# Kernel tuning notes

Measured on AMD Instinct MI355X. Metric: run time of the kernel, lower is better.

## Reference

```python
import jax, jax.numpy as jnp
import numpy as np

IN_CHANS = 64
OUT_CHANS = 64
IN_SHAPE = (128, 128)
RADIUS_CUTOFF = 0.03
KERNEL_SHAPE = (3, 4)  # (n_rings, n_phi) -> (3-1)*4+1 = 9 basis functions
EPS = 1e-5
NEG_SLOPE = 0.2


def _disco_basis():
    """Dynamically compile the DISCO filter basis on the (2H, 2W) equidistant grid.

    Returns psi of shape [K, kh, kw] (K=9 hat-function basis filters, including
    quadrature weight hx*hy) plus the pixel radii (Ry, Rx) of the support.
    All static -> constant-folded under jit.
    """
    H2, W2 = 2 * IN_SHAPE[0], 2 * IN_SHAPE[1]
    r_cut = RADIUS_CUTOFF / 2.0
    hy, hx = 1.0 / H2, 1.0 / W2            # normalized grid spacing
    Ry = int(np.ceil(r_cut / hy))
    Rx = int(np.ceil(r_cut / hx))
    dy = np.arange(-Ry, Ry + 1)[:, None] * hy
    dx = np.arange(-Rx, Rx + 1)[None, :] * hx
    r = np.sqrt(dy * dy + dx * dx)
    phi = np.arctan2(dy, dx) % (2.0 * np.pi)
    nr, nphi = KERNEL_SHAPE
    K = (nr - 1) * nphi + 1
    dr = r_cut / (nr - 1)
    dphi = 2.0 * np.pi / nphi
    ik = np.arange(K)[:, None, None]
    ir = np.where(ik > 0, (ik - 1) // nphi + 1, 0)   # radial ring index
    iphi = (ik - 1) % nphi                            # angular index
    # radial hat functions centered at ir*dr, clipped at the cutoff radius
    r_val = np.where((np.abs(r - ir * dr) <= dr) & (r <= r_cut),
                     1.0 - np.abs(r - ir * dr) / dr, 0.0)
    # periodic angular hat functions centered at iphi*dphi
    d_ang = np.abs(phi - iphi * dphi)
    d_ang = np.minimum(d_ang, 2.0 * np.pi - d_ang)
    phi_val = np.where(d_ang <= dphi, 1.0 - d_ang / dphi, 0.0)
    psi = np.where(ik == 0, r_val, r_val * phi_val)   # center basis is isotropic
    psi = psi * (hx * hy)                              # quadrature weight
    return jnp.asarray(psi, jnp.float32), Ry, Rx


def _upsample2x_align_corners(x):
    """Bilinear 2x upsample with align_corners=True, x: [N, C, H, W]."""
    N, C, H, W = x.shape

    def axis(n):
        no = 2 * n
        s = jnp.arange(no, dtype=jnp.float32) * (n - 1) / (no - 1)
        i0 = jnp.floor(s).astype(jnp.int32)
        i1 = jnp.minimum(i0 + 1, n - 1)
        w = (s - i0).astype(x.dtype)
        return i0, i1, w

    y0, y1, wy = axis(H)
    x = x[:, :, y0, :] * (1.0 - wy)[None, None, :, None] + x[:, :, y1, :] * wy[None, None, :, None]
    x0, x1, wx = axis(W)
    x = x[:, :, :, x0] * (1.0 - wx) + x[:, :, :, x1] * wx
    return x


def setup_inputs() -> dict:
    key = jax.random.key(0)
    k1, k2 = jax.random.split(key)
    image = jax.random.normal(k1, (4, IN_CHANS, IN_SHAPE[0], IN_SHAPE[1]), dtype=jnp.float32)
    K = (KERNEL_SHAPE[0] - 1) * KERNEL_SHAPE[1] + 1
    scale = 1.0 / np.sqrt(IN_CHANS * K)
    weight = jax.random.normal(k2, (OUT_CHANS, IN_CHANS, K), dtype=jnp.float32) * scale
    return {"image": image, "weight": weight}


def reference(image, weight):
    x = _upsample2x_align_corners(image)  # [N, Cin, 2H, 2W]
    # 2) DISCO conv: contract learned weights with compiled basis -> dense filter
    psi, Ry, Rx = _disco_basis()          # [K, kh, kw]
    kernel = jnp.einsum('oik,khw->oihw', weight, psi)
    y = jax.lax.conv_general_dilated(
        x, kernel, window_strides=(1, 1),
        padding=[(Ry, Ry), (Rx, Rx)],       # 'constant' zero padding, same size
        dimension_numbers=('NCHW', 'OIHW', 'NCHW'))
    # 3) InstanceNorm2d (affine=False, biased variance, eps=1e-5)
    mu = jnp.mean(y, axis=(2, 3), keepdims=True)
    var = jnp.var(y, axis=(2, 3), keepdims=True)
    y = (y - mu) * jax.lax.rsqrt(var + EPS)
    # 4) LeakyReLU(0.2)
    return jnp.where(y >= 0, y, NEG_SLOPE * y)
```

## Files before the change

kernel.cpp:

```cpp
#include <hip/hip_runtime.h>

#define NB 4
#define CIN 64
#define COUT 64
#define H 128
#define W 128
#define H2 256
#define W2 256
#define HSX 23
#define ZS 36

#define WS_W    0
#define WS_P1   32768
#define WS_P2   98304
#define WS_MU   163840
#define WS_RSTD 164096

constexpr double csqrt(double x) {
    double g = x > 1.0 ? x : 1.0;
    for (int i = 0; i < 64; ++i) g = 0.5 * (g + x / g);
    return g;
}
constexpr double catan_pos(double x) {
    double f = 1.0;
    for (int i = 0; i < 6; ++i) { x = x / (1.0 + csqrt(1.0 + x * x)); f *= 2.0; }
    double x2 = x * x, s = 0.0, term = x;
    for (int n = 0; n < 10; ++n) { s += term / (2 * n + 1) * ((n & 1) ? -1.0 : 1.0); term *= x2; }
    return f * s;
}
constexpr double catan2c(double y, double x) {
    const double PI = 3.141592653589793;
    if (x == 0.0 && y == 0.0) return 0.0;
    double ax = x < 0 ? -x : x, ay = y < 0 ? -y : y;
    double a = (ax >= ay) ? catan_pos(ay / ax) : (PI / 2.0 - catan_pos(ax / ay));
    if (x < 0) a = PI - a;
    return (y < 0) ? -a : a;
}

struct PsiTab { double v[81][9]; };
constexpr PsiTab compute_psi() {
    PsiTab P{};
    const double hy = 1.0 / 256.0;
    const double rcut = 0.015;
    const double dr = 0.0075;
    const double PI = 3.141592653589793;
    const double TWO_PI = 6.283185307179586;
    const double dphi = PI / 2.0;
    for (int ky = 0; ky < 9; ++ky)
        for (int kx = 0; kx < 9; ++kx) {
            double dy = (double)(ky - 4) * hy;
            double dx = (double)(kx - 4) * hy;
            double r = csqrt(dy * dy + dx * dx);
            double phi = catan2c(dy, dx);
            if (phi < 0.0) phi += TWO_PI;
            for (int k = 0; k < 9; ++k) {
                int ir = (k == 0) ? 0 : ((k - 1) / 4 + 1);
                double ctr = ir * dr;
                double ad = r > ctr ? r - ctr : ctr - r;
                double rv = (ad <= dr && r <= rcut) ? 1.0 - ad / dr : 0.0;
                double val;
                if (k == 0) val = rv;
                else {
                    int ip = (k - 1) % 4;
                    double da = phi - ip * dphi; if (da < 0) da = -da;
                    double d2 = TWO_PI - da; if (d2 < da) da = d2;
                    double pv = (da <= dphi) ? 1.0 - da / dphi : 0.0;
                    val = rv * pv;
                }
                P.v[ky * 9 + kx][k] = val * (hy * hy);
            }
        }
    return P;
}

struct TapTab {
    int nt;
    int off[48];
    float val[48][9];
    bool nz[48][9];
};
constexpr TapTab make_taps() {
    TapTab T{};
    PsiTab P = compute_psi();
    for (int ky = 0; ky < 9; ++ky)
        for (int kx = 0; kx < 9; ++kx) {
            int t = ky * 9 + kx;
            bool any = false;
            for (int k = 0; k < 9; ++k) if (P.v[t][k] != 0.0) any = true;
            if (!any) continue;
            int dy = ky - 4, dx = kx - 4;
            T.off[T.nt] = dy * HSX + dx;
            for (int k = 0; k < 9; ++k) {
                T.val[T.nt][k] = (float)P.v[t][k];
                T.nz[T.nt][k] = (P.v[t][k] != 0.0);
            }
            T.nt++;
        }
    return T;
}
constexpr TapTab TT = make_taps();
constexpr int NT = TT.nt;
static_assert(NT > 0 && NT <= 48, "tap table overflow");

using f32x2  = __attribute__((ext_vector_type(2))) float;
using f32x4  = __attribute__((ext_vector_type(4))) float;
using bf16x8 = __attribute__((ext_vector_type(8))) short;

__device__ __forceinline__ unsigned short f2bf_rne(float f) {
    unsigned u = __float_as_uint(f);
    unsigned r = (u + 0x7fff + ((u >> 16) & 1)) >> 16;
    return (unsigned short)r;
}
__device__ __forceinline__ unsigned pkrtz(float a, float b) {
    return (__float_as_uint(a) >> 16) | (__float_as_uint(b) & 0xffff0000u);
}

__global__ void setup_w(const float* __restrict__ wgt, float* __restrict__ ws) {
    unsigned short* wsW = (unsigned short*)(ws + WS_W);
    const int g = blockIdx.x;
    const int t = threadIdx.x;
    const int o = t >> 2;
    const int k0 = (t & 3) * 8;
#pragma unroll
    for (int j = 0; j < 8; ++j) {
        int kk = k0 + j;
        int ch = kk >> 4, k = kk & 15;
        float v = (k < 9) ? wgt[((size_t)o * CIN + 2 * g + ch) * 9 + k] : 0.f;
        wsW[g * 2048 + o * 32 + kk] = f2bf_rne(v);
    }
}

__global__ __launch_bounds__(256, 2) void conv_kernel(const float* __restrict__ img,
                                                      float* __restrict__ out,
                                                      float* __restrict__ ws) {
    __shared__ __align__(16) unsigned short zbuf[2][256][ZS];
    __shared__ f32x2 halo[2][22 * HSX];
    __shared__ f32x2 coarse[2][14 * 15];
    __shared__ float red1[4][64], red2[4][64];

    const int tid  = threadIdx.x;
    const int bid  = blockIdx.x;
    const int n    = bid >> 8;
    const int tile = bid & 255;
    const int ty0  = (tile >> 4) << 4;
    const int tx0  = (tile & 15) << 4;

    const int r = tid >> 4, c = tid & 15;
    const int hbase = (r + 3) * HSX + (c + 3);
    const int wv  = tid >> 6;
    const int l   = tid & 63;
    const int a16 = l & 15;
    const int kseg = (l >> 4) * 8;

    const unsigned short* wsW = (const unsigned short*)(ws + WS_W);

    {
        uint4* zr = (uint4*)&zbuf[0][0][0];
#pragma unroll
        for (int j = 0; j < 9; ++j) zr[tid + j * 256] = make_uint4(0, 0, 0, 0);
    }

    const float cs = 0.49803922f;

    int cy0 = (int)floorf((float)(ty0 - 3) * cs); cy0 = min(max(cy0, 0), 114);
    int cx0 = (int)floorf((float)(tx0 - 3) * cs); cx0 = min(max(cx0, 0), 114);

    const bool cok = tid < 196;
    const int ci = tid / 14, cj = tid - ci * 14;
    const int cgoff = (cy0 + ci) * W + (cx0 + cj);
    const int cwidx = ci * 15 + cj;
    float cv0 = 0.f, cv1 = 0.f;

    auto cload = [&](int g) {
        if (cok) {
            const float* b = img + ((size_t)n * CIN + 2 * g) * (H * W) + cgoff;
            cv0 = b[0];
            cv1 = b[H * W];
        }
    };
    auto cwrite = [&](int q) {
        if (cok) coarse[q][cwidx] = (f32x2){cv0, cv1};
    };

    unsigned fM[2];
    float fFY[2], fFX[2];
#pragma unroll
    for (int j = 0; j < 2; ++j) {
        int e = tid + j * 256;
        if (e < 484) {
            int hy = e / 22, hx = e - hy * 22;
            int uy = ty0 - 3 + hy, ux = tx0 - 3 + hx;
            unsigned zf = (((unsigned)uy >= 256u) || ((unsigned)ux >= 256u)) ? 1u : 0u;
            float syf = (float)uy * cs;
            float sxf = (float)ux * cs;
            int y0 = (int)floorf(syf);
            int x0 = (int)floorf(sxf);
            fFY[j] = syf - (float)y0;
            fFX[j] = sxf - (float)x0;
            int y0c = min(max(y0, 0), 127), x0c = min(max(x0, 0), 127);
            int dyo = min(y0c + 1, 127) - y0c;
            int dxo = min(x0c + 1, 127) - x0c;
            unsigned A = (unsigned)((y0c - cy0) * 15 + (x0c - cx0));
            fM[j] = A | ((unsigned)dxo << 9) | ((unsigned)dyo << 10) | (zf << 11)
                      | ((unsigned)(hy * HSX + hx) << 12);
        }
    }

    auto fine_build = [&](int q) {
#pragma unroll
        for (int j = 0; j < 2; ++j)
            if (tid < 484 - j * 256) {
                unsigned m = fM[j];
                const f32x2* cb = &coarse[q][0];
                int A = m & 511;
                int dxo = (m >> 9) & 1;
                int dyo = ((m >> 10) & 1) * 15;
                f32x2 c00 = cb[A],       c01 = cb[A + dxo];
                f32x2 c10 = cb[A + dyo], c11 = cb[A + dyo + dxo];
                f32x2 fyv = (f32x2){fFY[j], fFY[j]};
                f32x2 fxv = (f32x2){fFX[j], fFX[j]};
                f32x2 t0 = c00 + fyv * (c10 - c00);
                f32x2 t1 = c01 + fyv * (c11 - c01);
                f32x2 v  = t0 + fxv * (t1 - t0);
                if (m & (1u << 11)) v = (f32x2){0.f, 0.f};
                halo[q][m >> 12] = v;
            }
    };

    auto zphase = [&](int p) {
        const f32x2* hb = &halo[p][hbase - 72];
        f32x2 z[9];
#pragma unroll
        for (int k = 0; k < 9; ++k) z[k] = (f32x2){0.f, 0.f};
#pragma unroll
        for (int t = 0; t < NT; ++t) {
            f32x2 h = hb[72 + TT.off[t]];
#pragma unroll
            for (int k = 0; k < 9; ++k)
                if (TT.nz[t][k]) z[k] += h * TT.val[t][k];
        }
        unsigned short* zr = &zbuf[p][tid][0];
        ((uint2*)zr)[0] = make_uint2(pkrtz(z[0].x, z[1].x), pkrtz(z[2].x, z[3].x));
        ((uint2*)zr)[1] = make_uint2(pkrtz(z[4].x, z[5].x), pkrtz(z[6].x, z[7].x));
        zr[8] = (unsigned short)(__float_as_uint(z[8].x) >> 16);
        ((uint2*)(zr + 16))[0] = make_uint2(pkrtz(z[0].y, z[1].y), pkrtz(z[2].y, z[3].y));
        ((uint2*)(zr + 16))[1] = make_uint2(pkrtz(z[4].y, z[5].y), pkrtz(z[6].y, z[7].y));
        zr[24] = (unsigned short)(__float_as_uint(z[8].y) >> 16);
    };

    f32x4 acc[4][4];
#pragma unroll
    for (int m = 0; m < 4; ++m)
#pragma unroll
        for (int t = 0; t < 4; ++t) acc[m][t] = (f32x4){0.f, 0.f, 0.f, 0.f};

    cload(0); cwrite(0);
    __syncthreads();
    fine_build(0);
    cload(1);
    __syncthreads();
    cwrite(1);
    cload(2);
    __syncthreads();

#pragma unroll 1
    for (int i = 0; i <= 32; ++i) {
        if (i >= 1) {
            const int zp = (i - 1) & 1;
            bf16x8 af[4];
            const unsigned short* wp = wsW + (i - 1) * 2048 + a16 * 32 + kseg;
#pragma unroll
            for (int m = 0; m < 4; ++m)
                af[m] = *(const bf16x8*)(wp + m * 512);
            union { uint2 q2[2]; bf16x8 v; } bfr;
#pragma unroll
            for (int t = 0; t < 4; ++t) {
                const unsigned short* zp2 = &zbuf[zp][wv * 64 + t * 16 + a16][kseg];
                bfr.q2[0] = *(const uint2*)zp2;
                bfr.q2[1] = *(const uint2*)(zp2 + 4);
#pragma unroll
                for (int m = 0; m < 4; ++m)
                    acc[m][t] = __builtin_amdgcn_mfma_f32_16x16x32_bf16(af[m], bfr.v, acc[m][t], 0, 0, 0);
            }
        }
        if (i < 32)  zphase(i & 1);
        if (i <= 29) cwrite(i & 1);
        if (i <= 30) fine_build((i + 1) & 1);
        if (i <= 28) cload(i + 3);
        __syncthreads();
    }

#pragma unroll
    for (int m = 0; m < 4; ++m) {
#pragma unroll
        for (int r4 = 0; r4 < 4; ++r4) {
            float s = 0.f, q = 0.f;
#pragma unroll
            for (int t = 0; t < 4; ++t) {
                float v = acc[m][t][r4];
                s += v; q = fmaf(v, v, q);
            }
#pragma unroll
            for (int msk = 1; msk < 16; msk <<= 1) {
                s += __shfl_xor(s, msk);
                q += __shfl_xor(q, msk);
            }
            if (a16 == 0) {
                int o = m * 16 + (l >> 4) * 4 + r4;
                red1[wv][o] = s;
                red2[wv][o] = q;
            }
        }
    }

    const size_t nbase = (size_t)n * COUT * (H2 * W2);
#pragma unroll
    for (int m = 0; m < 4; ++m)
#pragma unroll
        for (int t = 0; t < 4; ++t) {
            int Y = ty0 + wv * 4 + t;
            int X = tx0 + a16;
#pragma unroll
            for (int r4 = 0; r4 < 4; ++r4) {
                int o = m * 16 + (l >> 4) * 4 + r4;
                out[nbase + (size_t)o * (H2 * W2) + Y * W2 + X] = acc[m][t][r4];
            }
        }
    __syncthreads();
    if (tid < 64) {
        float S1 = red1[0][tid] + red1[1][tid] + red1[2][tid] + red1[3][tid];
        float S2 = red2[0][tid] + red2[1][tid] + red2[2][tid] + red2[3][tid];
        ws[WS_P1 + (n * COUT + tid) * 256 + tile] = S1;
        ws[WS_P2 + (n * COUT + tid) * 256 + tile] = S2;
    }
}

__global__ void stats_kernel(float* __restrict__ ws) {
    const int co  = blockIdx.x;
    const int tid = threadIdx.x;
    float s1 = ws[WS_P1 + co * 256 + tid];
    float s2 = ws[WS_P2 + co * 256 + tid];
#pragma unroll
    for (int m = 1; m < 64; m <<= 1) { s1 += __shfl_xor(s1, m); s2 += __shfl_xor(s2, m); }
    __shared__ float r1[4], r2[4];
    if ((tid & 63) == 0) { r1[tid >> 6] = s1; r2[tid >> 6] = s2; }
    __syncthreads();
    if (tid == 0) {
        float S1 = r1[0] + r1[1] + r1[2] + r1[3];
        float S2 = r2[0] + r2[1] + r2[2] + r2[3];
        const float inv = 1.f / 65536.f;
        float mu  = S1 * inv;
        float var = S2 * inv - mu * mu;
        ws[WS_MU + co]   = mu;
        ws[WS_RSTD + co] = 1.f / sqrtf(var + 1e-5f);
    }
}

__global__ void norm_kernel(float* __restrict__ out, const float* __restrict__ ws) {
    const int total = NB * COUT * H2 * W2 / 4;
    for (int idx = blockIdx.x * blockDim.x + threadIdx.x; idx < total;
         idx += gridDim.x * blockDim.x) {
        int co = idx >> 14;
        float mu = ws[WS_MU + co];
        float rs = ws[WS_RSTD + co];
        float4 v = ((float4*)out)[idx];
        float* p = (float*)&v;
#pragma unroll
        for (int j = 0; j < 4; ++j) {
            float t = (p[j] - mu) * rs;
            p[j] = (t >= 0.f) ? t : 0.2f * t;
        }
        ((float4*)out)[idx] = v;
    }
}

extern "C" void kernel_launch(void* const* d_in, const int* in_sizes, int n_in,
                              void* d_out, int out_size, void* d_ws, size_t ws_size,
                              hipStream_t stream) {
    const float* img = (const float*)d_in[0];
    const float* wgt = (const float*)d_in[1];
    float* out = (float*)d_out;
    float* ws  = (float*)d_ws;

    setup_w<<<32, 256, 0, stream>>>(wgt, ws);
    conv_kernel<<<NB * 256, 256, 0, stream>>>(img, out, ws);
    stats_kernel<<<256, 256, 0, stream>>>(ws);
    norm_kernel<<<2048, 256, 0, stream>>>(out, ws);
}
```

Before: 153.2 us.

## Warp-specialize conv kernel into compute and producer wavefront groups

The conv block grows to 512 threads. Four wavefronts run the MFMA accumulation and z-phase basis projection, and four wavefronts load coarse input and build the upsampled halo. The aim is to take global loads and bilinear interpolation off the MFMA wavefronts' critical path so the two stages overlap. The cost is double the threads per block, which raises register and occupancy pressure under the new launch bounds, and block-wide syncs still tie the two groups together every iteration.

```diff
diff --git a/kernel.cpp b/kernel.cpp
--- a/kernel.cpp
+++ b/kernel.cpp
@@ -130,7 +130,7 @@
     }
 }
 
-__global__ __launch_bounds__(256, 2) void conv_kernel(const float* __restrict__ img,
+__global__ __launch_bounds__(512, 4) void conv_kernel(const float* __restrict__ img,
                                                       float* __restrict__ out,
                                                       float* __restrict__ ws) {
     __shared__ __align__(16) unsigned short zbuf[2][256][ZS];
@@ -145,19 +145,22 @@
     const int ty0  = (tile >> 4) << 4;
     const int tx0  = (tile & 15) << 4;
 
-    const int r = tid >> 4, c = tid & 15;
-    const int hbase = (r + 3) * HSX + (c + 3);
-    const int wv  = tid >> 6;
-    const int l   = tid & 63;
-    const int a16 = l & 15;
+    const int w    = tid >> 6;
+    const bool isC = (w < 4);
+    const int l    = tid & 63;
+    const int a16  = l & 15;
     const int kseg = (l >> 4) * 8;
+    const int mtid = tid & 255;
 
     const unsigned short* wsW = (const unsigned short*)(ws + WS_W);
 
     {
         uint4* zr = (uint4*)&zbuf[0][0][0];
 #pragma unroll
-        for (int j = 0; j < 9; ++j) zr[tid + j * 256] = make_uint4(0, 0, 0, 0);
+        for (int j = 0; j < 5; ++j) {
+            int idx = tid + j * 512;
+            if (idx < 2304) zr[idx] = make_uint4(0, 0, 0, 0);
+        }
     }
 
     const float cs = 0.49803922f;
@@ -165,11 +168,39 @@
     int cy0 = (int)floorf((float)(ty0 - 3) * cs); cy0 = min(max(cy0, 0), 114);
     int cx0 = (int)floorf((float)(tx0 - 3) * cs); cx0 = min(max(cx0, 0), 114);
 
-    const bool cok = tid < 196;
-    const int ci = tid / 14, cj = tid - ci * 14;
-    const int cgoff = (cy0 + ci) * W + (cx0 + cj);
-    const int cwidx = ci * 15 + cj;
+    bool cok = false;
+    int cgoff = 0, cwidx = 0;
     float cv0 = 0.f, cv1 = 0.f;
+    unsigned fM[2] = {0, 0};
+    float fFY[2] = {0.f, 0.f}, fFX[2] = {0.f, 0.f};
+
+    if (!isC) {
+        cok = mtid < 196;
+        int ci = mtid / 14, cj = mtid - ci * 14;
+        cgoff = (cy0 + ci) * W + (cx0 + cj);
+        cwidx = ci * 15 + cj;
+#pragma unroll
+        for (int j = 0; j < 2; ++j) {
+            int e = mtid + j * 256;
+            if (e < 484) {
+                int hy = e / 22, hx = e - hy * 22;
+                int uy = ty0 - 3 + hy, ux = tx0 - 3 + hx;
+                unsigned zf = (((unsigned)uy >= 256u) || ((unsigned)ux >= 256u)) ? 1u : 0u;
+                float syf = (float)uy * cs;
+                float sxf = (float)ux * cs;
+                int y0 = (int)floorf(syf);
+                int x0 = (int)floorf(sxf);
+                fFY[j] = syf - (float)y0;
+                fFX[j] = sxf - (float)x0;
+                int y0c = min(max(y0, 0), 127), x0c = min(max(x0, 0), 127);
+                int dyo = min(y0c + 1, 127) - y0c;
+                int dxo = min(x0c + 1, 127) - x0c;
+                unsigned A = (unsigned)((y0c - cy0) * 15 + (x0c - cx0));
+                fM[j] = A | ((unsigned)dxo << 9) | ((unsigned)dyo << 10) | (zf << 11)
+                          | ((unsigned)(hy * HSX + hx) << 12);
+            }
+        }
+    }
 
     auto cload = [&](int g) {
         if (cok) {
@@ -181,35 +212,10 @@
     auto cwrite = [&](int q) {
         if (cok) coarse[q][cwidx] = (f32x2){cv0, cv1};
     };
-
-    unsigned fM[2];
-    float fFY[2], fFX[2];
-#pragma unroll
-    for (int j = 0; j < 2; ++j) {
-        int e = tid + j * 256;
-        if (e < 484) {
-            int hy = e / 22, hx = e - hy * 22;
-            int uy = ty0 - 3 + hy, ux = tx0 - 3 + hx;
-            unsigned zf = (((unsigned)uy >= 256u) || ((unsigned)ux >= 256u)) ? 1u : 0u;
-            float syf = (float)uy * cs;
-            float sxf = (float)ux * cs;
-            int y0 = (int)floorf(syf);
-            int x0 = (int)floorf(sxf);
-            fFY[j] = syf - (float)y0;
-            fFX[j] = sxf - (float)x0;
-            int y0c = min(max(y0, 0), 127), x0c = min(max(x0, 0), 127);
-            int dyo = min(y0c + 1, 127) - y0c;
-            int dxo = min(x0c + 1, 127) - x0c;
-            unsigned A = (unsigned)((y0c - cy0) * 15 + (x0c - cx0));
-            fM[j] = A | ((unsigned)dxo << 9) | ((unsigned)dyo << 10) | (zf << 11)
-                      | ((unsigned)(hy * HSX + hx) << 12);
-        }
-    }
-
     auto fine_build = [&](int q) {
 #pragma unroll
         for (int j = 0; j < 2; ++j)
-            if (tid < 484 - j * 256) {
+            if (mtid < 484 - j * 256) {
                 unsigned m = fM[j];
                 const f32x2* cb = &coarse[q][0];
                 int A = m & 511;
@@ -227,6 +233,9 @@
             }
     };
 
+    const int r = mtid >> 4, c = mtid & 15;
+    const int hbase = (r + 3) * HSX + (c + 3);
+
     auto zphase = [&](int p) {
         const f32x2* hb = &halo[p][hbase - 72];
         f32x2 z[9];
@@ -239,7 +248,7 @@
             for (int k = 0; k < 9; ++k)
                 if (TT.nz[t][k]) z[k] += h * TT.val[t][k];
         }
-        unsigned short* zr = &zbuf[p][tid][0];
+        unsigned short* zr = &zbuf[p][mtid][0];
         ((uint2*)zr)[0] = make_uint2(pkrtz(z[0].x, z[1].x), pkrtz(z[2].x, z[3].x));
         ((uint2*)zr)[1] = make_uint2(pkrtz(z[4].x, z[5].x), pkrtz(z[6].x, z[7].x));
         zr[8] = (unsigned short)(__float_as_uint(z[8].x) >> 16);
@@ -254,78 +263,80 @@
 #pragma unroll
         for (int t = 0; t < 4; ++t) acc[m][t] = (f32x4){0.f, 0.f, 0.f, 0.f};
 
-    cload(0); cwrite(0);
+    if (!isC) { cload(0); cwrite(0); }
     __syncthreads();
-    fine_build(0);
-    cload(1);
+    if (!isC) { fine_build(0); cload(1); }
     __syncthreads();
-    cwrite(1);
-    cload(2);
+    if (!isC) { cwrite(1); cload(2); }
     __syncthreads();
 
 #pragma unroll 1
     for (int i = 0; i <= 32; ++i) {
-        if (i >= 1) {
-            const int zp = (i - 1) & 1;
-            bf16x8 af[4];
-            const unsigned short* wp = wsW + (i - 1) * 2048 + a16 * 32 + kseg;
-#pragma unroll
-            for (int m = 0; m < 4; ++m)
-                af[m] = *(const bf16x8*)(wp + m * 512);
-            union { uint2 q2[2]; bf16x8 v; } bfr;
+        if (isC) {
+            if (i >= 1) {
+                const int zp = (i - 1) & 1;
+                bf16x8 af[4];
+                const unsigned short* wp = wsW + (i - 1) * 2048 + a16 * 32 + kseg;
+#pragma unroll
+                for (int m = 0; m < 4; ++m)
+                    af[m] = *(const bf16x8*)(wp + m * 512);
+                union { uint2 q2[2]; bf16x8 v; } bfr;
+#pragma unroll
+                for (int t = 0; t < 4; ++t) {
+                    const unsigned short* zp2 = &zbuf[zp][w * 64 + t * 16 + a16][kseg];
+                    bfr.q2[0] = *(const uint2*)zp2;
+                    bfr.q2[1] = *(const uint2*)(zp2 + 4);
+#pragma unroll
+                    for (int m = 0; m < 4; ++m)
+                        acc[m][t] = __builtin_amdgcn_mfma_f32_16x16x32_bf16(af[m], bfr.v, acc[m][t], 0, 0, 0);
+                }
+            }
+            if (i < 32) zphase(i & 1);
+        } else {
+            if (i <= 29) cwrite(i & 1);
+            if (i <= 30) fine_build((i + 1) & 1);
+            if (i <= 28) cload(i + 3);
+        }
+        __syncthreads();
+    }
+
+    if (isC) {
+#pragma unroll
+        for (int m = 0; m < 4; ++m) {
+#pragma unroll
+            for (int r4 = 0; r4 < 4; ++r4) {
+                float s = 0.f, q = 0.f;
+#pragma unroll
+                for (int t = 0; t < 4; ++t) {
+                    float v = acc[m][t][r4];
+                    s += v; q = fmaf(v, v, q);
+                }
+#pragma unroll
+                for (int msk = 1; msk < 16; msk <<= 1) {
+                    s += __shfl_xor(s, msk);
+                    q += __shfl_xor(q, msk);
+                }
+                if (a16 == 0) {
+                    int o = m * 16 + (l >> 4) * 4 + r4;
+                    red1[w][o] = s;
+                    red2[w][o] = q;
+                }
+            }
+        }
+        const size_t nbase = (size_t)n * COUT * (H2 * W2);
+#pragma unroll
+        for (int m = 0; m < 4; ++m)
 #pragma unroll
             for (int t = 0; t < 4; ++t) {
-                const unsigned short* zp2 = &zbuf[zp][wv * 64 + t * 16 + a16][kseg];
-                bfr.q2[0] = *(const uint2*)zp2;
-                bfr.q2[1] = *(const uint2*)(zp2 + 4);
-#pragma unroll
-                for (int m = 0; m < 4; ++m)
-                    acc[m][t] = __builtin_amdgcn_mfma_f32_16x16x32_bf16(af[m], bfr.v, acc[m][t], 0, 0, 0);
-            }
-        }
-        if (i < 32)  zphase(i & 1);
-        if (i <= 29) cwrite(i & 1);
-        if (i <= 30) fine_build((i + 1) & 1);
-        if (i <= 28) cload(i + 3);
-        __syncthreads();
-    }
-
-#pragma unroll
-    for (int m = 0; m < 4; ++m) {
-#pragma unroll
-        for (int r4 = 0; r4 < 4; ++r4) {
-            float s = 0.f, q = 0.f;
-#pragma unroll
-            for (int t = 0; t < 4; ++t) {
-                float v = acc[m][t][r4];
-                s += v; q = fmaf(v, v, q);
-            }
-#pragma unroll
-            for (int msk = 1; msk < 16; msk <<= 1) {
-                s += __shfl_xor(s, msk);
-                q += __shfl_xor(q, msk);
-            }
-            if (a16 == 0) {
-                int o = m * 16 + (l >> 4) * 4 + r4;
-                red1[wv][o] = s;
-                red2[wv][o] = q;
-            }
-        }
-    }
-
-    const size_t nbase = (size_t)n * COUT * (H2 * W2);
-#pragma unroll
-    for (int m = 0; m < 4; ++m)
-#pragma unroll
-        for (int t = 0; t < 4; ++t) {
-            int Y = ty0 + wv * 4 + t;
-            int X = tx0 + a16;
-#pragma unroll
-            for (int r4 = 0; r4 < 4; ++r4) {
-                int o = m * 16 + (l >> 4) * 4 + r4;
-                out[nbase + (size_t)o * (H2 * W2) + Y * W2 + X] = acc[m][t][r4];
-            }
-        }
+                int Y = ty0 + w * 4 + t;
+                int X = tx0 + a16;
+#pragma unroll
+                for (int r4 = 0; r4 < 4; ++r4) {
+                    int o = m * 16 + (l >> 4) * 4 + r4;
+                    out[nbase + (size_t)o * (H2 * W2) + Y * W2 + X] = acc[m][t][r4];
+                }
+            }
+    }
     __syncthreads();
     if (tid < 64) {
         float S1 = red1[0][tid] + red1[1][tid] + red1[2][tid] + red1[3][tid];
@@ -383,7 +394,7 @@
     float* ws  = (float*)d_ws;
 
     setup_w<<<32, 256, 0, stream>>>(wgt, ws);
-    conv_kernel<<<NB * 256, 256, 0, stream>>>(img, out, ws);
+    conv_kernel<<<NB * 256, 512, 0, stream>>>(img, out, ws);
     stats_kernel<<<256, 256, 0, stream>>>(ws);
     norm_kernel<<<2048, 256, 0, stream>>>(out, ws);
 }
```

Result: slower. 443.3 us (+189.3%).
